# Performance work log

Hardware: AMD Instinct MI355X
Metric: run time of the kernel (lower is better)

Reference implementation:

```python
import jax, jax.numpy as jnp
import numpy as np

D, H, B = 512, 8, 64
NF, NO = 16384, 8192
EPS = 1e-5


def _ln(x):
    m = jnp.mean(x, axis=-1, keepdims=True)
    v = jnp.mean((x - m) ** 2, axis=-1, keepdims=True)
    return (x - m) / jnp.sqrt(v + EPS)


def setup_inputs() -> dict:
    key = jax.random.key(0)
    ks = jax.random.split(key, 16)
    s = 1.0 / np.sqrt(D)
    inp = {
        "hf": jax.random.normal(ks[0], (NF, D), jnp.float32),
        "ho": jax.random.normal(ks[1], (NO, D), jnp.float32),
        "ps": jax.random.normal(ks[2], (B, D), jnp.float32),
        "face_batch": jnp.sort(jax.random.randint(ks[3], (NF,), 0, B)),
        "obj_batch": jnp.sort(jax.random.randint(ks[4], (NO,), 0, B)),
        "Wq": jax.random.normal(ks[5], (D, D), jnp.float32) * s,
        "bq": jnp.zeros((D,), jnp.float32),
        "Wk": jax.random.normal(ks[6], (D, D), jnp.float32) * s,
        "bk": jnp.zeros((D,), jnp.float32),
        "Wv": jax.random.normal(ks[7], (D, D), jnp.float32) * s,
        "bv": jnp.zeros((D,), jnp.float32),
        "Wo": jax.random.normal(ks[8], (D, D), jnp.float32) * s,
        "bo": jnp.zeros((D,), jnp.float32),
        "Wg": jax.random.normal(ks[9], (D, D), jnp.float32) * s,
        "bg": jnp.full((D,), -1.0, jnp.float32),  # init.constant_(bias, -1.0)
        "alpha": jax.random.normal(ks[10], (D,), jnp.float32) * 0.1,
    }
    return inp


def reference(hf, ho, ps, face_batch, obj_batch, Wq, bq, Wk, bk, Wv, bv, Wo, bo, Wg, bg, alpha):
    dh = D // H
    nodes = jnp.concatenate([hf, ho], axis=0)            # (N, D)
    seg = jnp.concatenate([face_batch, obj_batch], 0)    # (N,)
    N = nodes.shape[0]

    # single-query cross-attention done as ragged/segment attention
    # (identical math to padded MHA with key_padding_mask)
    q = (ps @ Wq + bq).reshape(B, H, dh)                 # (B, H, dh)
    k = (nodes @ Wk + bk).reshape(N, H, dh)
    v = (nodes @ Wv + bv).reshape(N, H, dh)

    scores = jnp.einsum("nhd,nhd->nh", k, q[seg]) / np.sqrt(dh)   # (N, H)
    mx = jax.ops.segment_max(scores, seg, num_segments=B)          # (B, H)
    e = jnp.exp(scores - mx[seg])                                  # (N, H)
    denom = jax.ops.segment_sum(e, seg, num_segments=B)            # (B, H)
    num = jax.ops.segment_sum(e[:, :, None] * v, seg, num_segments=B)  # (B, H, dh)
    attn = (num / denom[:, :, None]).reshape(B, D)
    attn_out = attn @ Wo + bo

    fs = _ln(ps + attn_out)                               # (B, D)
    gate = jax.nn.sigmoid(hf @ Wg + bg)                   # (NF, D)
    signal = alpha * fs[face_batch]                       # (NF, D)
    hf_new = _ln(hf + gate * signal)
    return hf_new, fs
```

## Files before the change

### kernel.cpp

```cpp
#include <hip/hip_runtime.h>
#include <hip/hip_bf16.h>
#include <math.h>

constexpr int D  = 512;
constexpr int H  = 8;
constexpr int DH = 64;
constexpr int B  = 64;
constexpr int NF = 16384;
constexpr int NO = 8192;
constexpr int NT = NF + NO;
constexpr float EPS = 1e-5f;
constexpr float LOG2E = 1.4426950408889634f;

typedef short short8 __attribute__((ext_vector_type(8)));
typedef float f32x4 __attribute__((ext_vector_type(4)));
typedef unsigned short ushort;
typedef ushort ushort8v __attribute__((ext_vector_type(8)));
typedef ushort ushort4v __attribute__((ext_vector_type(4)));

__device__ __forceinline__ ushort f2bf(float f) {
  unsigned int x = __float_as_uint(f);
  x += 0x7FFF + ((x >> 16) & 1);
  return (ushort)(x >> 16);
}
__device__ __forceinline__ float bf2f(ushort u) {
  return __uint_as_float(((unsigned int)u) << 16);
}
__device__ __forceinline__ float fast_exp(float x) {
  return __builtin_amdgcn_exp2f(x * LOG2E);
}
__device__ __forceinline__ float fast_sigmoid(float z) {
  return __builtin_amdgcn_rcpf(1.0f + __builtin_amdgcn_exp2f(-z * LOG2E));
}

__global__ __launch_bounds__(256) void k_qproj(const float* __restrict__ ps,
                                               const float* __restrict__ Wq,
                                               const float* __restrict__ bq,
                                               float* __restrict__ q) {
  __shared__ float row[D];
  int b = blockIdx.x, cg = blockIdx.y, t = threadIdx.x;
  for (int i = t; i < D; i += 256) row[i] = ps[(size_t)b * D + i];
  __syncthreads();
  int col = cg * 64 + (t >> 2), eq = t & 3;
  float acc = 0.f;
  const float* wp = Wq + (size_t)(eq * 128) * D + col;
  #pragma unroll 8
  for (int e = 0; e < 128; ++e) acc += row[eq * 128 + e] * wp[(size_t)e * D];
  acc += __shfl_xor(acc, 1); acc += __shfl_xor(acc, 2);
  if (eq == 0) q[(size_t)b * D + col] = acc + bq[col];
}

__global__ __launch_bounds__(256) void k_pkproj(const float* __restrict__ q,
                                                const float* __restrict__ Wk,
                                                const float* __restrict__ bk,
                                                float* __restrict__ Pk,
                                                float* __restrict__ qbk) {
  int b = blockIdx.x, h = blockIdx.y;
  __shared__ float qs[DH];
  __shared__ float bks[DH];
  int t = threadIdx.x;
  if (t < DH) { qs[t] = q[b * D + h * DH + t]; bks[t] = bk[h * DH + t]; }
  __syncthreads();
  for (int e = t; e < D; e += 256) {
    float acc = 0.f;
    #pragma unroll 8
    for (int j = 0; j < DH; ++j) acc += Wk[(size_t)e * D + h * DH + j] * qs[j];
    Pk[((size_t)b * H + h) * D + e] = acc;
  }
  if (t == 0) {
    float s = 0.f;
    for (int j = 0; j < DH; ++j) s += bks[j] * qs[j];
    qbk[b * H + h] = s;
  }
}

__global__ void k_bounds(const int* __restrict__ fb, const int* __restrict__ ob,
                         int* __restrict__ fstart, int* __restrict__ ostart) {
  int t = threadIdx.x;
  if (t <= B) {
    int lo = 0, hi = NF;
    while (lo < hi) { int mid = (lo + hi) >> 1; if (fb[mid] < t) lo = mid + 1; else hi = mid; }
    fstart[t] = lo;
  } else if (t >= 128 && t <= 128 + B) {
    int v = t - 128;
    int lo = 0, hi = NO;
    while (lo < hi) { int mid = (lo + hi) >> 1; if (ob[mid] < v) lo = mid + 1; else hi = mid; }
    ostart[v] = lo;
  }
}

__global__ __launch_bounds__(256) void k_scores(const float* __restrict__ hf,
                                                const float* __restrict__ ho,
                                                const int* __restrict__ fb,
                                                const int* __restrict__ ob,
                                                const float* __restrict__ Pk,
                                                const float* __restrict__ qbk,
                                                float* __restrict__ scores) {
  int lane = threadIdx.x & 63;
  int n = blockIdx.x * 4 + (threadIdx.x >> 6);
  int b; const float* row;
  if (n < NF) { b = fb[n]; row = hf + (size_t)n * D; }
  else        { b = ob[n - NF]; row = ho + (size_t)(n - NF) * D; }
  const float4* r4 = (const float4*)row;
  float4 x0 = r4[lane * 2], x1 = r4[lane * 2 + 1];
  float acc[H];
  #pragma unroll
  for (int h = 0; h < H; ++h) {
    const float4* p4 = (const float4*)(Pk + ((size_t)b * H + h) * D) + lane * 2;
    float4 p0 = p4[0], p1 = p4[1];
    acc[h] = x0.x * p0.x + x0.y * p0.y + x0.z * p0.z + x0.w * p0.w +
             x1.x * p1.x + x1.y * p1.y + x1.z * p1.z + x1.w * p1.w;
  }
  #pragma unroll
  for (int h = 0; h < H; ++h) {
    float v = acc[h];
    #pragma unroll
    for (int off = 32; off; off >>= 1) v += __shfl_xor(v, off);
    if (lane == h) scores[(size_t)n * H + h] = (v + qbk[b * H + h]) * 0.125f;
  }
}

__global__ __launch_bounds__(512) void k_segsoftmax(const float* __restrict__ scores,
                                                    const int* __restrict__ fstart,
                                                    const int* __restrict__ ostart,
                                                    float* __restrict__ evals,
                                                    float* __restrict__ denom) {
  int b = blockIdx.x;
  int h = threadIdx.x >> 6, lane = threadIdx.x & 63;
  int f0 = fstart[b], f1 = fstart[b + 1];
  int o0 = ostart[b], o1 = ostart[b + 1];
  float m = -1e30f;
  for (int i = f0 + lane; i < f1; i += 64) m = fmaxf(m, scores[(size_t)i * H + h]);
  for (int i = o0 + lane; i < o1; i += 64) m = fmaxf(m, scores[(size_t)(NF + i) * H + h]);
  #pragma unroll
  for (int off = 32; off; off >>= 1) m = fmaxf(m, __shfl_xor(m, off));
  float s = 0.f;
  for (int i = f0 + lane; i < f1; i += 64) {
    float e = fast_exp(scores[(size_t)i * H + h] - m);
    evals[(size_t)i * H + h] = e; s += e;
  }
  for (int i = o0 + lane; i < o1; i += 64) {
    float e = fast_exp(scores[(size_t)(NF + i) * H + h] - m);
    evals[(size_t)(NF + i) * H + h] = e; s += e;
  }
  #pragma unroll
  for (int off = 32; off; off >>= 1) s += __shfl_xor(s, off);
  if (lane == 0) denom[b * H + h] = s;
}

__global__ __launch_bounds__(512) void k_Taccum(const float* __restrict__ hf,
                                                const float* __restrict__ ho,
                                                const int* __restrict__ fstart,
                                                const int* __restrict__ ostart,
                                                const float* __restrict__ evals,
                                                float* __restrict__ T) {
  int b = blockIdx.x, chunk = blockIdx.y;
  int e = threadIdx.x;
  int f0 = fstart[b], flen = fstart[b + 1] - f0;
  int o0 = ostart[b], olen = ostart[b + 1] - o0;
  int L = flen + olen;
  float acc[8] = {0.f, 0.f, 0.f, 0.f, 0.f, 0.f, 0.f, 0.f};
  for (int idx = chunk; idx < L; idx += 8) {
    int n; const float* row;
    if (idx < flen) { n = f0 + idx; row = hf + (size_t)n * D; }
    else            { n = NF + o0 + (idx - flen); row = ho + (size_t)(o0 + idx - flen) * D; }
    float x = row[e];
    const float4* ev = (const float4*)(evals + (size_t)n * H);
    float4 e0 = ev[0], e1 = ev[1];
    acc[0] += e0.x * x; acc[1] += e0.y * x; acc[2] += e0.z * x; acc[3] += e0.w * x;
    acc[4] += e1.x * x; acc[5] += e1.y * x; acc[6] += e1.z * x; acc[7] += e1.w * x;
  }
  #pragma unroll
  for (int h = 0; h < H; ++h) atomicAdd(&T[((size_t)b * H + h) * D + e], acc[h]);
}

__global__ __launch_bounds__(256) void k_attn(const float* __restrict__ T,
                                              const float* __restrict__ denom,
                                              const float* __restrict__ Wv,
                                              const float* __restrict__ bv,
                                              float* __restrict__ attn) {
  __shared__ float Ts[D];
  int b = blockIdx.x, h = blockIdx.y, t = threadIdx.x;
  for (int i = t; i < D; i += 256) Ts[i] = T[((size_t)b * H + h) * D + i];
  __syncthreads();
  int col = h * DH + (t >> 2), eq = t & 3;
  float acc = 0.f;
  const float* wp = Wv + (size_t)(eq * 128) * D + col;
  #pragma unroll 8
  for (int e = 0; e < 128; ++e) acc += Ts[eq * 128 + e] * wp[(size_t)e * D];
  acc += __shfl_xor(acc, 1); acc += __shfl_xor(acc, 2);
  if (eq == 0) attn[(size_t)b * D + col] = acc / denom[b * H + h] + bv[col];
}

__global__ __launch_bounds__(256) void k_x(const float* __restrict__ attn,
                                           const float* __restrict__ Wo,
                                           const float* __restrict__ bo,
                                           const float* __restrict__ ps,
                                           float* __restrict__ x) {
  __shared__ float As[D];
  int b = blockIdx.x, cg = blockIdx.y, t = threadIdx.x;
  for (int i = t; i < D; i += 256) As[i] = attn[(size_t)b * D + i];
  __syncthreads();
  int col = cg * 64 + (t >> 2), eq = t & 3;
  float acc = 0.f;
  const float* wp = Wo + (size_t)(eq * 128) * D + col;
  #pragma unroll 8
  for (int e = 0; e < 128; ++e) acc += As[eq * 128 + e] * wp[(size_t)e * D];
  acc += __shfl_xor(acc, 1); acc += __shfl_xor(acc, 2);
  if (eq == 0) x[(size_t)b * D + col] = acc + bo[col] + ps[(size_t)b * D + col];
}

__global__ __launch_bounds__(512) void k_ln(const float* __restrict__ x,
                                            float* __restrict__ fs) {
  __shared__ float redS[8], redQ[8];
  __shared__ float sM, sI;
  int b = blockIdx.x, t = threadIdx.x;
  float v = x[(size_t)b * D + t];
  float s = v, sq = v * v;
  #pragma unroll
  for (int off = 32; off; off >>= 1) { s += __shfl_xor(s, off); sq += __shfl_xor(sq, off); }
  int wv = t >> 6, ln = t & 63;
  if (ln == 0) { redS[wv] = s; redQ[wv] = sq; }
  __syncthreads();
  if (t == 0) {
    float S = 0.f, Q = 0.f;
    #pragma unroll
    for (int i = 0; i < 8; ++i) { S += redS[i]; Q += redQ[i]; }
    float mean = S * (1.f / D);
    float var = Q * (1.f / D) - mean * mean;
    sM = mean; sI = rsqrtf(var + EPS);
  }
  __syncthreads();
  fs[(size_t)b * D + t] = (v - sM) * sI;
}

__global__ __launch_bounds__(256) void k_prepW(const float* __restrict__ Wg,
                                               ushort* __restrict__ Wgt) {
  __shared__ float tile[32][33];
  int bx = blockIdx.x, by = blockIdx.y;
  int tx = threadIdx.x & 31, ty = threadIdx.x >> 5;
  #pragma unroll
  for (int i = 0; i < 4; ++i)
    tile[ty + i * 8][tx] = Wg[(size_t)(by * 32 + ty + i * 8) * D + bx * 32 + tx];
  __syncthreads();
  #pragma unroll
  for (int i = 0; i < 4; ++i)
    Wgt[(size_t)(bx * 32 + ty + i * 8) * D + by * 32 + tx] = f2bf(tile[tx][ty + i * 8]);
}

__global__ __launch_bounds__(512) void k_gate_ln(const float* __restrict__ hf,
                                                 const ushort* __restrict__ Wgt,
                                                 const float* __restrict__ bg,
                                                 const float* __restrict__ alpha,
                                                 const float* __restrict__ fs,
                                                 const int* __restrict__ fb,
                                                 float* __restrict__ out) {
  __shared__ ushort Asb[2][64][40];
  __shared__ ushort gls[64][544];
  const int tid = threadIdx.x;
  const int lane = tid & 63, w = tid >> 6;
  const int rowBase = blockIdx.x * 64;
  const int lrow = lane & 15, kg = lane >> 4;

  const int arow = tid >> 3, akq = tid & 7;
  const float* Agp = hf + (size_t)(rowBase + arow) * D + akq * 4;
  {
    float4 f = *(const float4*)Agp;
    ushort4v u = { f2bf(f.x), f2bf(f.y), f2bf(f.z), f2bf(f.w) };
    *(ushort4v*)&Asb[0][arow][akq * 4] = u;
  }
  __syncthreads();

  f32x4 acc[4][4] = {};
  const ushort* Bp = Wgt + (size_t)(w * 64 + lrow) * D + kg * 8;

  for (int step = 0; step < 16; ++step) {
    int cur = step & 1;
    if (step < 15) {
      float4 f = *(const float4*)(Agp + (step + 1) * 32);
      ushort4v u = { f2bf(f.x), f2bf(f.y), f2bf(f.z), f2bf(f.w) };
      *(ushort4v*)&Asb[cur ^ 1][arow][akq * 4] = u;
    }
    short8 a[4], bfr[4];
    #pragma unroll
    for (int m = 0; m < 4; ++m)
      a[m] = *(const short8*)&Asb[cur][lrow + m * 16][kg * 8];
    #pragma unroll
    for (int n = 0; n < 4; ++n)
      bfr[n] = *(const short8*)(Bp + (size_t)n * 16 * D + step * 32);
    #pragma unroll
    for (int m = 0; m < 4; ++m)
      #pragma unroll
      for (int n = 0; n < 4; ++n)
        acc[m][n] = __builtin_amdgcn_mfma_f32_16x16x32_bf16(a[m], bfr[n], acc[m][n], 0, 0, 0);
    __syncthreads();
  }

  #pragma unroll
  for (int n = 0; n < 4; ++n) {
    int col = w * 64 + n * 16 + lrow;
    float bgv = bg[col];
    int sblk = (col >> 3) ^ w;
    #pragma unroll
    for (int m = 0; m < 4; ++m) {
      #pragma unroll
      for (int r = 0; r < 4; ++r) {
        int rib = m * 16 + kg * 4 + r;
        float g = fast_sigmoid(acc[m][n][r] + bgv);
        ((ushort*)gls)[rib * 544 + sblk * 8 + (lrow & 7)] = f2bf(g);
      }
    }
  }
  __syncthreads();

  const int row = tid >> 3, cg = tid & 7;
  const int grow = rowBase + row;
  const int bidx = fb[grow];
  const float* hfr = hf + (size_t)grow * D + cg * 64;
  const float* fsr = fs + (size_t)bidx * D + cg * 64;
  const float* alr = alpha + cg * 64;
  float x[64];
  float s = 0.f, sq = 0.f;
  #pragma unroll
  for (int jb = 0; jb < 8; ++jb) {
    int sblk = (cg * 8 + jb) ^ cg;
    union { ushort8v v; ushort u[8]; } ug;
    ug.v = *(const ushort8v*)((const ushort*)gls + row * 544 + sblk * 8);
    float4 h0 = *(const float4*)(hfr + jb * 8);
    float4 h1 = *(const float4*)(hfr + jb * 8 + 4);
    float4 p0 = *(const float4*)(fsr + jb * 8);
    float4 p1 = *(const float4*)(fsr + jb * 8 + 4);
    float4 a0 = *(const float4*)(alr + jb * 8);
    float4 a1 = *(const float4*)(alr + jb * 8 + 4);
    float hv[8] = {h0.x, h0.y, h0.z, h0.w, h1.x, h1.y, h1.z, h1.w};
    float pv[8] = {p0.x, p0.y, p0.z, p0.w, p1.x, p1.y, p1.z, p1.w};
    float av[8] = {a0.x, a0.y, a0.z, a0.w, a1.x, a1.y, a1.z, a1.w};
    #pragma unroll
    for (int i = 0; i < 8; ++i) {
      float xv = hv[i] + bf2f(ug.u[i]) * (av[i] * pv[i]);
      x[jb * 8 + i] = xv; s += xv; sq += xv * xv;
    }
  }
  #pragma unroll
  for (int off = 1; off < 8; off <<= 1) { s += __shfl_xor(s, off); sq += __shfl_xor(sq, off); }
  float mean = s * (1.f / D);
  float inv = rsqrtf(sq * (1.f / D) - mean * mean + EPS);
  float* op = out + (size_t)grow * D + cg * 64;
  #pragma unroll
  for (int j4 = 0; j4 < 16; ++j4) {
    float4 o = { (x[j4 * 4 + 0] - mean) * inv, (x[j4 * 4 + 1] - mean) * inv,
                 (x[j4 * 4 + 2] - mean) * inv, (x[j4 * 4 + 3] - mean) * inv };
    *(float4*)(op + j4 * 4) = o;
  }
}

extern "C" void kernel_launch(void* const* d_in, const int* in_sizes, int n_in,
                              void* d_out, int out_size, void* d_ws, size_t ws_size,
                              hipStream_t stream) {
  const float* hf    = (const float*)d_in[0];
  const float* ho    = (const float*)d_in[1];
  const float* ps    = (const float*)d_in[2];
  const int*   fb    = (const int*)d_in[3];
  const int*   ob    = (const int*)d_in[4];
  const float* Wq    = (const float*)d_in[5];
  const float* bq    = (const float*)d_in[6];
  const float* Wk    = (const float*)d_in[7];
  const float* bk    = (const float*)d_in[8];
  const float* Wv    = (const float*)d_in[9];
  const float* bv    = (const float*)d_in[10];
  const float* Wo    = (const float*)d_in[11];
  const float* bo    = (const float*)d_in[12];
  const float* Wg    = (const float*)d_in[13];
  const float* bg    = (const float*)d_in[14];
  const float* alpha = (const float*)d_in[15];

  float* out    = (float*)d_out;
  float* fs_out = out + (size_t)NF * D;

  ushort* Wgt   = (ushort*)d_ws;
  float* ws     = (float*)d_ws + (512 * 512 * 2) / 4;
  float* q      = ws;
  float* Pk     = q + B * D;
  float* qbk    = Pk + B * H * D;
  float* scores = qbk + B * H;
  float* evals  = scores + (size_t)NT * H;
  float* denom  = evals + (size_t)NT * H;
  float* T      = denom + B * H;
  float* attn   = T + B * H * D;
  float* xbuf   = attn + B * D;
  int* fstart   = (int*)(xbuf + B * D);
  int* ostart   = fstart + (B + 1);

  k_prepW<<<dim3(16, 16), 256, 0, stream>>>(Wg, Wgt);
  k_qproj<<<dim3(B, 8), 256, 0, stream>>>(ps, Wq, bq, q);
  k_pkproj<<<dim3(B, H), 256, 0, stream>>>(q, Wk, bk, Pk, qbk);
  k_bounds<<<1, 256, 0, stream>>>(fb, ob, fstart, ostart);
  hipMemsetAsync(T, 0, (size_t)B * H * D * sizeof(float), stream);
  k_scores<<<NT / 4, 256, 0, stream>>>(hf, ho, fb, ob, Pk, qbk, scores);
  k_segsoftmax<<<B, 512, 0, stream>>>(scores, fstart, ostart, evals, denom);
  k_Taccum<<<dim3(B, 8), 512, 0, stream>>>(hf, ho, fstart, ostart, evals, T);
  k_attn<<<dim3(B, H), 256, 0, stream>>>(T, denom, Wv, bv, attn);
  k_x<<<dim3(B, 8), 256, 0, stream>>>(attn, Wo, bo, ps, xbuf);
  k_ln<<<B, 512, 0, stream>>>(xbuf, fs_out);
  k_gate_ln<<<NF / 64, 512, 0, stream>>>(hf, Wgt, bg, alpha, fs_out, fb, out);
}
```

Before: 162.1 us.

## Fuse attention output, projection and layernorm; retile gate GEMM with register prefetch

Result: slower. 183.5 us (+13.2%).

```diff
diff --git a/kernel.cpp b/kernel.cpp
--- a/kernel.cpp
+++ b/kernel.cpp
@@ -174,49 +174,49 @@
   for (int h = 0; h < H; ++h) atomicAdd(&T[((size_t)b * H + h) * D + e], acc[h]);
 }
 
-__global__ __launch_bounds__(256) void k_attn(const float* __restrict__ T,
-                                              const float* __restrict__ denom,
-                                              const float* __restrict__ Wv,
-                                              const float* __restrict__ bv,
-                                              float* __restrict__ attn) {
-  __shared__ float Ts[D];
-  int b = blockIdx.x, h = blockIdx.y, t = threadIdx.x;
-  for (int i = t; i < D; i += 256) Ts[i] = T[((size_t)b * H + h) * D + i];
-  __syncthreads();
-  int col = h * DH + (t >> 2), eq = t & 3;
-  float acc = 0.f;
-  const float* wp = Wv + (size_t)(eq * 128) * D + col;
-  #pragma unroll 8
-  for (int e = 0; e < 128; ++e) acc += Ts[eq * 128 + e] * wp[(size_t)e * D];
-  acc += __shfl_xor(acc, 1); acc += __shfl_xor(acc, 2);
-  if (eq == 0) attn[(size_t)b * D + col] = acc / denom[b * H + h] + bv[col];
-}
-
-__global__ __launch_bounds__(256) void k_x(const float* __restrict__ attn,
-                                           const float* __restrict__ Wo,
-                                           const float* __restrict__ bo,
-                                           const float* __restrict__ ps,
-                                           float* __restrict__ x) {
-  __shared__ float As[D];
-  int b = blockIdx.x, cg = blockIdx.y, t = threadIdx.x;
-  for (int i = t; i < D; i += 256) As[i] = attn[(size_t)b * D + i];
-  __syncthreads();
-  int col = cg * 64 + (t >> 2), eq = t & 3;
-  float acc = 0.f;
-  const float* wp = Wo + (size_t)(eq * 128) * D + col;
-  #pragma unroll 8
-  for (int e = 0; e < 128; ++e) acc += As[eq * 128 + e] * wp[(size_t)e * D];
-  acc += __shfl_xor(acc, 1); acc += __shfl_xor(acc, 2);
-  if (eq == 0) x[(size_t)b * D + col] = acc + bo[col] + ps[(size_t)b * D + col];
-}
-
-__global__ __launch_bounds__(512) void k_ln(const float* __restrict__ x,
-                                            float* __restrict__ fs) {
+__global__ __launch_bounds__(512) void k_attn_x_ln(const float* __restrict__ T,
+                                                   const float* __restrict__ denom,
+                                                   const float* __restrict__ Wv,
+                                                   const float* __restrict__ bv,
+                                                   const float* __restrict__ Wo,
+                                                   const float* __restrict__ bo,
+                                                   const float* __restrict__ ps,
+                                                   float* __restrict__ fs_out) {
+  __shared__ float Ts[H * D];
+  __shared__ float attn[D];
   __shared__ float redS[8], redQ[8];
   __shared__ float sM, sI;
   int b = blockIdx.x, t = threadIdx.x;
-  float v = x[(size_t)b * D + t];
-  float s = v, sq = v * v;
+  for (int i = t; i < H * D; i += 512) Ts[i] = T[(size_t)b * H * D + i];
+  __syncthreads();
+  {
+    int c = t, h = c >> 6;
+    const float* tp = Ts + h * D;
+    float a0 = 0.f, a1 = 0.f, a2 = 0.f, a3 = 0.f;
+    #pragma unroll 4
+    for (int e = 0; e < D; e += 4) {
+      a0 += tp[e + 0] * Wv[(size_t)(e + 0) * D + c];
+      a1 += tp[e + 1] * Wv[(size_t)(e + 1) * D + c];
+      a2 += tp[e + 2] * Wv[(size_t)(e + 2) * D + c];
+      a3 += tp[e + 3] * Wv[(size_t)(e + 3) * D + c];
+    }
+    attn[c] = (a0 + a1 + a2 + a3) / denom[b * H + h] + bv[c];
+  }
+  __syncthreads();
+  float xv;
+  {
+    int c = t;
+    float a0 = bo[c] + ps[(size_t)b * D + c], a1 = 0.f, a2 = 0.f, a3 = 0.f;
+    #pragma unroll 4
+    for (int e = 0; e < D; e += 4) {
+      a0 += attn[e + 0] * Wo[(size_t)(e + 0) * D + c];
+      a1 += attn[e + 1] * Wo[(size_t)(e + 1) * D + c];
+      a2 += attn[e + 2] * Wo[(size_t)(e + 2) * D + c];
+      a3 += attn[e + 3] * Wo[(size_t)(e + 3) * D + c];
+    }
+    xv = a0 + a1 + a2 + a3;
+  }
+  float s = xv, sq = xv * xv;
   #pragma unroll
   for (int off = 32; off; off >>= 1) { s += __shfl_xor(s, off); sq += __shfl_xor(sq, off); }
   int wv = t >> 6, ln = t & 63;
@@ -231,7 +231,7 @@
     sM = mean; sI = rsqrtf(var + EPS);
   }
   __syncthreads();
-  fs[(size_t)b * D + t] = (v - sM) * sI;
+  fs_out[(size_t)b * D + t] = (xv - sM) * sI;
 }
 
 __global__ __launch_bounds__(256) void k_prepW(const float* __restrict__ Wg,
@@ -248,66 +248,77 @@
     Wgt[(size_t)(bx * 32 + ty + i * 8) * D + by * 32 + tx] = f2bf(tile[tx][ty + i * 8]);
 }
 
-__global__ __launch_bounds__(512) void k_gate_ln(const float* __restrict__ hf,
+__global__ __launch_bounds__(256) void k_gate_ln(const float* __restrict__ hf,
                                                  const ushort* __restrict__ Wgt,
                                                  const float* __restrict__ bg,
                                                  const float* __restrict__ alpha,
                                                  const float* __restrict__ fs,
                                                  const int* __restrict__ fb,
                                                  float* __restrict__ out) {
-  __shared__ ushort Asb[2][64][40];
-  __shared__ ushort gls[64][544];
+  __shared__ ushort Asb[2][32][40];
+  __shared__ ushort gls[32][544];
   const int tid = threadIdx.x;
   const int lane = tid & 63, w = tid >> 6;
-  const int rowBase = blockIdx.x * 64;
+  const int rowBase = blockIdx.x * 32;
   const int lrow = lane & 15, kg = lane >> 4;
 
   const int arow = tid >> 3, akq = tid & 7;
   const float* Agp = hf + (size_t)(rowBase + arow) * D + akq * 4;
+  const ushort* Bp = Wgt + (size_t)(w * 128 + lrow) * D + kg * 8;
+
+  float4 fA[2];
+  short8 bb[2][8];
   {
-    float4 f = *(const float4*)Agp;
-    ushort4v u = { f2bf(f.x), f2bf(f.y), f2bf(f.z), f2bf(f.w) };
+    float4 f0 = *(const float4*)Agp;
+    ushort4v u = { f2bf(f0.x), f2bf(f0.y), f2bf(f0.z), f2bf(f0.w) };
     *(ushort4v*)&Asb[0][arow][akq * 4] = u;
   }
-  __syncthreads();
-
-  f32x4 acc[4][4] = {};
-  const ushort* Bp = Wgt + (size_t)(w * 64 + lrow) * D + kg * 8;
-
+  fA[1] = *(const float4*)(Agp + 32);
+  fA[0] = *(const float4*)(Agp + 64);
+  #pragma unroll
+  for (int n = 0; n < 8; ++n) bb[0][n] = *(const short8*)(Bp + (size_t)n * 16 * D);
+  __syncthreads();
+
+  f32x4 acc[2][8] = {};
+  #pragma unroll
   for (int step = 0; step < 16; ++step) {
-    int cur = step & 1;
+    const int cur = step & 1;
     if (step < 15) {
-      float4 f = *(const float4*)(Agp + (step + 1) * 32);
+      #pragma unroll
+      for (int n = 0; n < 8; ++n)
+        bb[cur ^ 1][n] = *(const short8*)(Bp + (size_t)n * 16 * D + (step + 1) * 32);
+    }
+    short8 a0 = *(const short8*)&Asb[cur][lrow][kg * 8];
+    short8 a1 = *(const short8*)&Asb[cur][lrow + 16][kg * 8];
+    #pragma unroll
+    for (int n = 0; n < 8; ++n)
+      acc[0][n] = __builtin_amdgcn_mfma_f32_16x16x32_bf16(a0, bb[cur][n], acc[0][n], 0, 0, 0);
+    #pragma unroll
+    for (int n = 0; n < 8; ++n)
+      acc[1][n] = __builtin_amdgcn_mfma_f32_16x16x32_bf16(a1, bb[cur][n], acc[1][n], 0, 0, 0);
+    if (step < 15) {
+      float4 f = fA[(step + 1) & 1];
       ushort4v u = { f2bf(f.x), f2bf(f.y), f2bf(f.z), f2bf(f.w) };
       *(ushort4v*)&Asb[cur ^ 1][arow][akq * 4] = u;
-    }
-    short8 a[4], bfr[4];
-    #pragma unroll
-    for (int m = 0; m < 4; ++m)
-      a[m] = *(const short8*)&Asb[cur][lrow + m * 16][kg * 8];
-    #pragma unroll
-    for (int n = 0; n < 4; ++n)
-      bfr[n] = *(const short8*)(Bp + (size_t)n * 16 * D + step * 32);
-    #pragma unroll
-    for (int m = 0; m < 4; ++m)
-      #pragma unroll
-      for (int n = 0; n < 4; ++n)
-        acc[m][n] = __builtin_amdgcn_mfma_f32_16x16x32_bf16(a[m], bfr[n], acc[m][n], 0, 0, 0);
+      if (step < 13)
+        fA[(step + 1) & 1] = *(const float4*)(Agp + (step + 3) * 32);
+    }
     __syncthreads();
   }
 
   #pragma unroll
-  for (int n = 0; n < 4; ++n) {
-    int col = w * 64 + n * 16 + lrow;
+  for (int n = 0; n < 8; ++n) {
+    int col = w * 128 + n * 16 + lrow;
     float bgv = bg[col];
-    int sblk = (col >> 3) ^ w;
-    #pragma unroll
-    for (int m = 0; m < 4; ++m) {
+    int colblk = col >> 3;
+    int sblk = colblk ^ (colblk >> 3);
+    #pragma unroll
+    for (int m = 0; m < 2; ++m) {
       #pragma unroll
       for (int r = 0; r < 4; ++r) {
         int rib = m * 16 + kg * 4 + r;
         float g = fast_sigmoid(acc[m][n][r] + bgv);
-        ((ushort*)gls)[rib * 544 + sblk * 8 + (lrow & 7)] = f2bf(g);
+        ((ushort*)gls)[rib * 544 + sblk * 8 + (col & 7)] = f2bf(g);
       }
     }
   }
@@ -386,9 +397,7 @@
   float* evals  = scores + (size_t)NT * H;
   float* denom  = evals + (size_t)NT * H;
   float* T      = denom + B * H;
-  float* attn   = T + B * H * D;
-  float* xbuf   = attn + B * D;
-  int* fstart   = (int*)(xbuf + B * D);
+  int* fstart   = (int*)(T + B * H * D);
   int* ostart   = fstart + (B + 1);
 
   k_prepW<<<dim3(16, 16), 256, 0, stream>>>(Wg, Wgt);
@@ -399,8 +408,6 @@
   k_scores<<<NT / 4, 256, 0, stream>>>(hf, ho, fb, ob, Pk, qbk, scores);
   k_segsoftmax<<<B, 512, 0, stream>>>(scores, fstart, ostart, evals, denom);
   k_Taccum<<<dim3(B, 8), 512, 0, stream>>>(hf, ho, fstart, ostart, evals, T);
-  k_attn<<<dim3(B, H), 256, 0, stream>>>(T, denom, Wv, bv, attn);
-  k_x<<<dim3(B, 8), 256, 0, stream>>>(attn, Wo, bo, ps, xbuf);
-  k_ln<<<B, 512, 0, stream>>>(xbuf, fs_out);
-  k_gate_ln<<<NF / 64, 512, 0, stream>>>(hf, Wgt, bg, alpha, fs_out, fb, out);
-}
+  k_attn_x_ln<<<B, 512, 0, stream>>>(T, denom, Wv, bv, Wo, bo, ps, fs_out);
+  k_gate_ln<<<NF / 32, 256, 0, stream>>>(hf, Wgt, bg, alpha, fs_out, fb, out);
+}
```

## Restructure gate GEMM to load A directly into registers with smaller blocks

Applied to the files above, without the earlier changes.

Result: slower. 194.2 us (+19.8%).

```diff
diff --git a/kernel.cpp b/kernel.cpp
--- a/kernel.cpp
+++ b/kernel.cpp
@@ -16,7 +16,6 @@
 typedef float f32x4 __attribute__((ext_vector_type(4)));
 typedef unsigned short ushort;
 typedef ushort ushort8v __attribute__((ext_vector_type(8)));
-typedef ushort ushort4v __attribute__((ext_vector_type(4)));
 
 __device__ __forceinline__ ushort f2bf(float f) {
   unsigned int x = __float_as_uint(f);
@@ -31,6 +30,14 @@
 }
 __device__ __forceinline__ float fast_sigmoid(float z) {
   return __builtin_amdgcn_rcpf(1.0f + __builtin_amdgcn_exp2f(-z * LOG2E));
+}
+__device__ __forceinline__ short8 cvt8(float4 f0, float4 f1) {
+  union { short8 v; __hip_bfloat162 h[4]; } u;
+  u.h[0] = __float22bfloat162_rn(float2{f0.x, f0.y});
+  u.h[1] = __float22bfloat162_rn(float2{f0.z, f0.w});
+  u.h[2] = __float22bfloat162_rn(float2{f1.x, f1.y});
+  u.h[3] = __float22bfloat162_rn(float2{f1.z, f1.w});
+  return u.v;
 }
 
 __global__ __launch_bounds__(256) void k_qproj(const float* __restrict__ ps,
@@ -248,66 +255,54 @@
     Wgt[(size_t)(bx * 32 + ty + i * 8) * D + by * 32 + tx] = f2bf(tile[tx][ty + i * 8]);
 }
 
-__global__ __launch_bounds__(512) void k_gate_ln(const float* __restrict__ hf,
-                                                 const ushort* __restrict__ Wgt,
-                                                 const float* __restrict__ bg,
-                                                 const float* __restrict__ alpha,
-                                                 const float* __restrict__ fs,
-                                                 const int* __restrict__ fb,
-                                                 float* __restrict__ out) {
-  __shared__ ushort Asb[2][64][40];
-  __shared__ ushort gls[64][544];
+__global__ __launch_bounds__(256, 4) void k_gate_ln(const float* __restrict__ hf,
+                                                    const ushort* __restrict__ Wgt,
+                                                    const float* __restrict__ bg,
+                                                    const float* __restrict__ alpha,
+                                                    const float* __restrict__ fs,
+                                                    const int* __restrict__ fb,
+                                                    float* __restrict__ out) {
+  __shared__ ushort gls[32][544];
   const int tid = threadIdx.x;
   const int lane = tid & 63, w = tid >> 6;
-  const int rowBase = blockIdx.x * 64;
+  const int rowBase = blockIdx.x * 32;
   const int lrow = lane & 15, kg = lane >> 4;
 
-  const int arow = tid >> 3, akq = tid & 7;
-  const float* Agp = hf + (size_t)(rowBase + arow) * D + akq * 4;
-  {
-    float4 f = *(const float4*)Agp;
-    ushort4v u = { f2bf(f.x), f2bf(f.y), f2bf(f.z), f2bf(f.w) };
-    *(ushort4v*)&Asb[0][arow][akq * 4] = u;
-  }
-  __syncthreads();
-
-  f32x4 acc[4][4] = {};
-  const ushort* Bp = Wgt + (size_t)(w * 64 + lrow) * D + kg * 8;
-
+  const float*  Ap = hf  + (size_t)(rowBase + lrow) * D + kg * 8;
+  const ushort* Bp = Wgt + (size_t)(w * 128 + lrow) * D + kg * 8;
+
+  f32x4 acc[2][8] = {};
+  #pragma unroll 4
   for (int step = 0; step < 16; ++step) {
-    int cur = step & 1;
-    if (step < 15) {
-      float4 f = *(const float4*)(Agp + (step + 1) * 32);
-      ushort4v u = { f2bf(f.x), f2bf(f.y), f2bf(f.z), f2bf(f.w) };
-      *(ushort4v*)&Asb[cur ^ 1][arow][akq * 4] = u;
+    short8 a[2], b[8];
+    #pragma unroll
+    for (int m = 0; m < 2; ++m) {
+      const float* p = Ap + (size_t)m * 16 * D + step * 32;
+      a[m] = cvt8(*(const float4*)p, *(const float4*)(p + 4));
     }
-    short8 a[4], bfr[4];
-    #pragma unroll
-    for (int m = 0; m < 4; ++m)
-      a[m] = *(const short8*)&Asb[cur][lrow + m * 16][kg * 8];
-    #pragma unroll
-    for (int n = 0; n < 4; ++n)
-      bfr[n] = *(const short8*)(Bp + (size_t)n * 16 * D + step * 32);
-    #pragma unroll
-    for (int m = 0; m < 4; ++m)
+    #pragma unroll
+    for (int n = 0; n < 8; ++n)
+      b[n] = *(const short8*)(Bp + (size_t)n * 16 * D + step * 32);
+    #pragma unroll
+    for (int m = 0; m < 2; ++m)
       #pragma unroll
-      for (int n = 0; n < 4; ++n)
-        acc[m][n] = __builtin_amdgcn_mfma_f32_16x16x32_bf16(a[m], bfr[n], acc[m][n], 0, 0, 0);
-    __syncthreads();
-  }
-
-  #pragma unroll
-  for (int n = 0; n < 4; ++n) {
-    int col = w * 64 + n * 16 + lrow;
+      for (int n = 0; n < 8; ++n)
+        acc[m][n] = __builtin_amdgcn_mfma_f32_16x16x32_bf16(a[m], b[n], acc[m][n], 0, 0, 0);
+  }
+
+  #pragma unroll
+  for (int n = 0; n < 8; ++n) {
+    int col = w * 128 + n * 16 + lrow;
     float bgv = bg[col];
-    int sblk = (col >> 3) ^ w;
-    #pragma unroll
-    for (int m = 0; m < 4; ++m) {
+    int colblk = col >> 3;
+    int sblk = colblk ^ (colblk >> 3);
+    #pragma unroll
+    for (int m = 0; m < 2; ++m) {
       #pragma unroll
       for (int r = 0; r < 4; ++r) {
         int rib = m * 16 + kg * 4 + r;
         float g = fast_sigmoid(acc[m][n][r] + bgv);
-        ((ushort*)gls)[rib * 544 + sblk * 8 + (lrow & 7)] = f2bf(g);
+        ((ushort*)gls)[rib * 544 + sblk * 8 + (col & 7)] = f2bf(g);
       }
     }
   }
@@ -402,5 +397,5 @@
   k_attn<<<dim3(B, H), 256, 0, stream>>>(T, denom, Wv, bv, attn);
   k_x<<<dim3(B, 8), 256, 0, stream>>>(attn, Wo, bo, ps, xbuf);
   k_ln<<<B, 512, 0, stream>>>(xbuf, fs_out);
-  k_gate_ln<<<NF / 64, 512, 0, stream>>>(hf, Wgt, bg, alpha, fs_out, fb, out);
-}
+  k_gate_ln<<<NF / 32, 256, 0, stream>>>(hf, Wgt, bg, alpha, fs_out, fb, out);
+}
```
